# Performance work log

Measured on AMD Instinct MI355X. Metric: run time of the kernel, lower is better.

## Reference

```python
import jax, jax.numpy as jnp
import numpy as np

N_FFT = 1024
HOP = 256
B = 8
T = 2048  # n_frames
FREQ = N_FFT // 2 + 1


def setup_inputs() -> dict:
    key = jax.random.key(0)
    k1, k2 = jax.random.split(key)
    real_stft = jax.random.normal(k1, (B, 1, T, FREQ), dtype=jnp.float32)
    imag_stft = jax.random.normal(k2, (B, 1, T, FREQ), dtype=jnp.float32)
    # Build DFT synthesis matrices (same as torch module __init__, scaled=False)
    n = np.arange(N_FFT)
    hann = (0.5 - 0.5 * np.cos(2.0 * np.pi * n / N_FFT))  # fftbins=True hann
    ang = 2.0 * np.pi * np.outer(n, n) / N_FFT            # [k, n]
    W_real = (np.cos(ang) * hann[None, :] / N_FFT).astype(np.float32)
    W_imag = (np.sin(ang) * hann[None, :] / N_FFT).astype(np.float32)
    ola_window = (hann ** 2).astype(np.float32)
    return {
        "real_stft": real_stft,
        "imag_stft": imag_stft,
        "W_real": jnp.asarray(W_real),
        "W_imag": jnp.asarray(W_imag),
        "ola_window": jnp.asarray(ola_window),
    }


def reference(real_stft, imag_stft, W_real, W_imag, ola_window):
    n_fft = W_real.shape[0]
    b, _, n_frames, _ = real_stft.shape
    # (B, T, F) -> (B, F, T)
    fr = jnp.swapaxes(real_stft[:, 0], 1, 2)
    fi = jnp.swapaxes(imag_stft[:, 0], 1, 2)
    # Hermitian extension to full spectrum (B, n_fft, T)
    full_r = jnp.concatenate([fr, jnp.flip(fr[:, 1:-1, :], axis=1)], axis=1)
    full_i = jnp.concatenate([fi, -jnp.flip(fi[:, 1:-1, :], axis=1)], axis=1)
    # 1x1-conv DFT projection: out[b,t,n] = sum_k W[k,n] * x[b,k,t]
    frames = (jnp.einsum('kn,bkt->btn', W_real, full_r)
              - jnp.einsum('kn,bkt->btn', W_imag, full_i))  # (B, T, n_fft)
    out_len = (n_frames - 1) * HOP + n_fft
    # Overlap-add fold via scatter-add
    idx = (jnp.arange(n_frames)[:, None] * HOP + jnp.arange(n_fft)[None, :]).reshape(-1)
    y = jnp.zeros((b, out_len), frames.dtype).at[:, idx].add(frames.reshape(b, -1))
    # Window-sum fold + normalization
    wsum = jnp.zeros((out_len,), frames.dtype).at[idx].add(jnp.tile(ola_window, n_frames))
    wsum = jnp.clip(wsum, 1e-11, None)
    y = y / wsum[None, :]
    half = n_fft // 2
    return y[:, half:out_len - half]
```

## Files before the change

### kernel.cpp

```cpp
#include <hip/hip_runtime.h>


#define BATCH    8
#define NFRAMES  2048
#define FREQ     513
#define OUTCOLS  524032
#define FRAMES_B ((size_t)16384 * 1024 * 2)
#define TW_OFF   FRAMES_B
#define WS_NEED  (FRAMES_B + 1024 * 8)

#define PD(a) ((a) + ((a) >> 4))

typedef __attribute__((ext_vector_type(2))) float f32x2;

__device__ __forceinline__ unsigned short f2bf(float x) {
    unsigned u = __float_as_uint(x);
    return (unsigned short)((u + 0x7fffu + ((u >> 16) & 1u)) >> 16);
}

__global__ __launch_bounds__(256) void twiddle_prep(float* __restrict__ tw) {
    int k = blockIdx.x * 256 + threadIdx.x;
    float s, c;
    sincosf(6.283185307179586f * (float)k * (1.0f / 1024.0f), &s, &c);
    ((f32x2*)tw)[k] = (f32x2){c, s};
}

__global__ __launch_bounds__(256) void ifft_frames3(
    const float* __restrict__ re, const float* __restrict__ im,
    const float* __restrict__ ola, const float* __restrict__ twg,
    unsigned short* __restrict__ frames) {
    __shared__ f32x2 X[1088], Y[1088];

    const int blk = blockIdx.x;
    const int r0  = blk * 2;
    const int tid = threadIdx.x;
    const f32x2* tw = (const f32x2*)twg;

    const float* fre0 = re + (size_t)r0 * FREQ;
    const float* fim0 = im + (size_t)r0 * FREQ;
    const float* fre1 = fre0 + FREQ;
    const float* fim1 = fim0 + FREQ;
#pragma unroll
    for (int h = 0; h < 2; ++h) {
        int k = tid + 256 * h;
        float a1 = fre0[k], b1 = fim0[k];
        float a2 = fre1[k], b2 = fim1[k];
        if (k == 0) { b1 = 0.0f; b2 = 0.0f; }
        X[PD(k)] = (f32x2){a1 - b2, b1 + a2};
        if (k > 0) X[PD(1024 - k)] = (f32x2){a1 + b2, a2 - b1};
    }
    if (tid == 0)
        X[PD(512)] = (f32x2){fre0[512], fre1[512]};
    __syncthreads();

#define STAGE(S, RB, WB)                                                      \
    {                                                                         \
        const int p  = tid / (S);                                             \
        const int q  = tid % (S);                                             \
        f32x2 a = RB[PD(tid)];                                                \
        f32x2 b = RB[PD(tid + 256)];                                          \
        f32x2 c = RB[PD(tid + 512)];                                          \
        f32x2 d = RB[PD(tid + 768)];                                          \
        float apcr = a[0] + c[0], apci = a[1] + c[1];                         \
        float amcr = a[0] - c[0], amci = a[1] - c[1];                         \
        float bpdr = b[0] + d[0], bpdi = b[1] + d[1];                         \
        float jbr  = -(b[1] - d[1]), jbi = (b[0] - d[0]);        \
        const int t1 = p * (S);                                               \
        f32x2 w1 = tw[t1], w2 = tw[2 * t1], w3 = tw[3 * t1];                  \
        const int wb = 4 * (S) * p + q;                                       \
        WB[PD(wb)] = (f32x2){apcr + bpdr, apci + bpdi};                       \
        float u1r = amcr + jbr, u1i = amci + jbi;                             \
        WB[PD(wb + (S))]     = (f32x2){u1r * w1[0] - u1i * w1[1],             \
                                       u1r * w1[1] + u1i * w1[0]};            \
        float u2r = apcr - bpdr, u2i = apci - bpdi;                           \
        WB[PD(wb + 2 * (S))] = (f32x2){u2r * w2[0] - u2i * w2[1],             \
                                       u2r * w2[1] + u2i * w2[0]};            \
        float u3r = amcr - jbr, u3i = amci - jbi;                             \
        WB[PD(wb + 3 * (S))] = (f32x2){u3r * w3[0] - u3i * w3[1],             \
                                       u3r * w3[1] + u3i * w3[0]};            \
        __syncthreads();                                                      \
    }

    STAGE(1,  X, Y)
    STAGE(4,  Y, X)
    STAGE(16, X, Y)
    STAGE(64, Y, X)
    {
        f32x2 a = X[PD(tid)];
        f32x2 b = X[PD(tid + 256)];
        f32x2 c = X[PD(tid + 512)];
        f32x2 d = X[PD(tid + 768)];
        float apcr = a[0] + c[0], apci = a[1] + c[1];
        float amcr = a[0] - c[0], amci = a[1] - c[1];
        float bpdr = b[0] + d[0], bpdi = b[1] + d[1];
        float jbr  = -(b[1] - d[1]), jbi = (b[0] - d[0]);
        Y[PD(tid)]       = (f32x2){apcr + bpdr, apci + bpdi};
        Y[PD(tid + 256)] = (f32x2){amcr + jbr, amci + jbi};
        Y[PD(tid + 512)] = (f32x2){apcr - bpdr, apci - bpdi};
        Y[PD(tid + 768)] = (f32x2){amcr - jbr, amci - jbi};
        __syncthreads();
    }
#undef STAGE

    const float inv = 1.0f / 1024.0f;
    unsigned* f0 = (unsigned*)frames + (size_t)r0 * 512;
    unsigned* f1 = f0 + 512;
#pragma unroll
    for (int h = 0; h < 2; ++h) {
        int n = 2 * tid + 512 * h;
        f32x2 o  = *(const f32x2*)(ola + n);
        float s0 = sqrtf(o[0]) * inv, s1 = sqrtf(o[1]) * inv;
        f32x2 z0 = Y[PD(n)], z1 = Y[PD(n + 1)];
        f0[tid + 256 * h] = (unsigned)f2bf(z0[0] * s0) | ((unsigned)f2bf(z1[0] * s1) << 16);
        f1[tid + 256 * h] = (unsigned)f2bf(z0[1] * s0) | ((unsigned)f2bf(z1[1] * s1) << 16);
    }
}

__global__ __launch_bounds__(256) void ola_fold2(
    const unsigned short* __restrict__ frames, const float* __restrict__ ola,
    float* __restrict__ out) {
    const int col0 = (blockIdx.x * 256 + threadIdx.x) * 2;
    if (col0 >= OUTCOLS) return;
    const int b  = blockIdx.y;
    const int s  = col0 + 512;
    const int g  = s >> 8;
    const int ls = s & 255;

    float acc0 = 0.0f, acc1 = 0.0f, ws0 = 0.0f, ws1 = 0.0f;
#pragma unroll
    for (int j = 0; j < 4; ++j) {
        const int t = g - j;
        if (t >= 0 && t < NFRAMES) {
            unsigned u = *(const unsigned*)(frames + ((size_t)(b * NFRAMES + t) << 10) + ls + 256 * j);
            acc0 += __uint_as_float(u << 16);
            acc1 += __uint_as_float(u & 0xffff0000u);
            f32x2 o = *(const f32x2*)(ola + ls + 256 * j);
            ws0 += o[0];
            ws1 += o[1];
        }
    }
    ws0 = fmaxf(ws0, 1e-11f);
    ws1 = fmaxf(ws1, 1e-11f);
    *(f32x2*)(out + (size_t)b * OUTCOLS + col0) = (f32x2){acc0 / ws0, acc1 / ws1};
}

__global__ __launch_bounds__(256) void istft_naive(
    const float* __restrict__ re, const float* __restrict__ im,
    const float* __restrict__ Wr, const float* __restrict__ Wi,
    const float* __restrict__ ola, float* __restrict__ out) {
    const int g = blockIdx.x + 2, b = blockIdx.y, ls = threadIdx.x;
    __shared__ float s_fr[4][FREQ];
    __shared__ float s_fi[4][FREQ];
#pragma unroll
    for (int jj = 0; jj < 4; ++jj) {
        const int t = g - jj;
        const bool valid = (t >= 0 && t < NFRAMES);
        const size_t base = ((size_t)b * NFRAMES + (valid ? t : 0)) * FREQ;
        for (int k = ls; k < FREQ; k += 256) {
            const float f = (k == 0 || k == FREQ - 1) ? 1.0f : 2.0f;
            s_fr[jj][k] = valid ? re[base + k] * f : 0.0f;
            s_fi[jj][k] = valid ? im[base + k] * f : 0.0f;
        }
    }
    __syncthreads();
    const float* wr = Wr + ls;
    const float* wi = Wi + ls;
    float acc = 0.0f;
    for (int k = 0; k < FREQ; ++k) {
        const float* wrk = wr + (size_t)k * 1024;
        const float* wik = wi + (size_t)k * 1024;
#pragma unroll
        for (int jj = 0; jj < 4; ++jj) {
            acc = fmaf(wrk[jj * 256], s_fr[jj][k], acc);
            acc = fmaf(-wik[jj * 256], s_fi[jj][k], acc);
        }
    }
    float wsv = 0.0f;
#pragma unroll
    for (int jj = 0; jj < 4; ++jj) {
        const int t = g - jj;
        if (t >= 0 && t < NFRAMES) wsv += ola[ls + jj * 256];
    }
    wsv = fmaxf(wsv, 1e-11f);
    out[(size_t)b * OUTCOLS + (g * 256 + ls - 512)] = acc / wsv;
}

extern "C" void kernel_launch(void* const* d_in, const int* in_sizes, int n_in,
                              void* d_out, int out_size, void* d_ws, size_t ws_size,
                              hipStream_t stream) {
    const float* re  = (const float*)d_in[0];
    const float* im  = (const float*)d_in[1];
    const float* Wr  = (const float*)d_in[2];
    const float* Wi  = (const float*)d_in[3];
    const float* ola = (const float*)d_in[4];
    float* out = (float*)d_out;

    if (ws_size >= WS_NEED) {
        unsigned short* frames = (unsigned short*)d_ws;
        float* tw = (float*)((char*)d_ws + TW_OFF);
        hipLaunchKernelGGL(twiddle_prep, dim3(4), dim3(256), 0, stream, tw);
        hipLaunchKernelGGL(ifft_frames3, dim3(8192), dim3(256), 0, stream,
                           re, im, ola, tw, frames);
        hipLaunchKernelGGL(ola_fold2, dim3(1024, BATCH), dim3(256), 0, stream,
                           frames, ola, out);
    } else {
        dim3 grid(2047, BATCH);
        hipLaunchKernelGGL(istft_naive, grid, dim3(256), 0, stream,
                           re, im, Wr, Wi, ola, out);
    }
}
```

Measured before the change: 46.19 us.

## Fuse Hermitian load into first FFT stage, write output directly, widen OLA fold

The Hermitian-extension load now feeds the first radix-4 butterfly straight from registers, which removes one shared-memory round trip and a barrier. The final butterfly writes bf16 frame outputs directly instead of staging them through shared memory, also dropping a barrier. The overlap-add fold now handles four columns per thread with 8-byte and 16-byte vector loads and a half-size grid. Frame stores become 2-byte scattered writes instead of packed 4-byte writes, which may reduce store efficiency.

```diff
diff --git a/kernel.cpp b/kernel.cpp
--- a/kernel.cpp
+++ b/kernel.cpp
@@ -12,6 +12,8 @@
 #define PD(a) ((a) + ((a) >> 4))
 
 typedef __attribute__((ext_vector_type(2))) float f32x2;
+typedef __attribute__((ext_vector_type(4))) float f32x4;
+typedef __attribute__((ext_vector_type(2))) unsigned uint2v;
 
 __device__ __forceinline__ unsigned short f2bf(float x) {
     unsigned u = __float_as_uint(x);
@@ -25,14 +27,13 @@
     ((f32x2*)tw)[k] = (f32x2){c, s};
 }
 
-__global__ __launch_bounds__(256) void ifft_frames3(
+__global__ __launch_bounds__(256) void ifft_frames5(
     const float* __restrict__ re, const float* __restrict__ im,
     const float* __restrict__ ola, const float* __restrict__ twg,
     unsigned short* __restrict__ frames) {
     __shared__ f32x2 X[1088], Y[1088];
 
-    const int blk = blockIdx.x;
-    const int r0  = blk * 2;
+    const int r0  = blockIdx.x * 2;
     const int tid = threadIdx.x;
     const f32x2* tw = (const f32x2*)twg;
 
@@ -40,23 +41,54 @@
     const float* fim0 = im + (size_t)r0 * FREQ;
     const float* fre1 = fre0 + FREQ;
     const float* fim1 = fim0 + FREQ;
-#pragma unroll
-    for (int h = 0; h < 2; ++h) {
-        int k = tid + 256 * h;
-        float a1 = fre0[k], b1 = fim0[k];
-        float a2 = fre1[k], b2 = fim1[k];
-        if (k == 0) { b1 = 0.0f; b2 = 0.0f; }
-        X[PD(k)] = (f32x2){a1 - b2, b1 + a2};
-        if (k > 0) X[PD(1024 - k)] = (f32x2){a1 + b2, a2 - b1};
-    }
-    if (tid == 0)
-        X[PD(512)] = (f32x2){fre0[512], fre1[512]};
+
+    {
+        f32x2 a, b, c, d;
+        {
+            float A1 = fre0[tid], B1 = fim0[tid];
+            float A2 = fre1[tid], B2 = fim1[tid];
+            if (tid == 0) { B1 = 0.0f; B2 = 0.0f; }
+            a = (f32x2){A1 - B2, B1 + A2};
+        }
+        {
+            float A1 = fre0[tid + 256], B1 = fim0[tid + 256];
+            float A2 = fre1[tid + 256], B2 = fim1[tid + 256];
+            b = (f32x2){A1 - B2, B1 + A2};
+        }
+        {
+            int m = 512 - tid;
+            float A1 = fre0[m], B1 = fim0[m];
+            float A2 = fre1[m], B2 = fim1[m];
+            if (tid == 0) { B1 = 0.0f; B2 = 0.0f; }
+            c = (f32x2){A1 + B2, A2 - B1};
+        }
+        {
+            int m = 256 - tid;
+            float A1 = fre0[m], B1 = fim0[m];
+            float A2 = fre1[m], B2 = fim1[m];
+            d = (f32x2){A1 + B2, A2 - B1};
+        }
+        float apcr = a[0] + c[0], apci = a[1] + c[1];
+        float amcr = a[0] - c[0], amci = a[1] - c[1];
+        float bpdr = b[0] + d[0], bpdi = b[1] + d[1];
+        float jbr  = -(b[1] - d[1]), jbi = (b[0] - d[0]);
+        f32x2 w1 = tw[tid], w2 = tw[2 * tid], w3 = tw[3 * tid];
+        const int wb = 4 * tid;
+        Y[PD(wb)] = (f32x2){apcr + bpdr, apci + bpdi};
+        float u1r = amcr + jbr, u1i = amci + jbi;
+        Y[PD(wb + 1)] = (f32x2){u1r * w1[0] - u1i * w1[1], u1r * w1[1] + u1i * w1[0]};
+        float u2r = apcr - bpdr, u2i = apci - bpdi;
+        Y[PD(wb + 2)] = (f32x2){u2r * w2[0] - u2i * w2[1], u2r * w2[1] + u2i * w2[0]};
+        float u3r = amcr - jbr, u3i = amci - jbi;
+        Y[PD(wb + 3)] = (f32x2){u3r * w3[0] - u3i * w3[1], u3r * w3[1] + u3i * w3[0]};
+    }
     __syncthreads();
 
 #define STAGE(S, RB, WB)                                                      \
     {                                                                         \
-        const int p  = tid / (S);                                             \
-        const int q  = tid % (S);                                             \
+        const int S_ = (S);                                                   \
+        const int p  = tid / S_;                                              \
+        const int q  = tid - p * S_;                                          \
         f32x2 a = RB[PD(tid)];                                                \
         f32x2 b = RB[PD(tid + 256)];                                          \
         f32x2 c = RB[PD(tid + 512)];                                          \
@@ -65,26 +97,27 @@
         float amcr = a[0] - c[0], amci = a[1] - c[1];                         \
         float bpdr = b[0] + d[0], bpdi = b[1] + d[1];                         \
         float jbr  = -(b[1] - d[1]), jbi = (b[0] - d[0]);        \
-        const int t1 = p * (S);                                               \
+        const int t1 = p * S_;                                                \
         f32x2 w1 = tw[t1], w2 = tw[2 * t1], w3 = tw[3 * t1];                  \
-        const int wb = 4 * (S) * p + q;                                       \
+        const int wb = 4 * S_ * p + q;                                        \
         WB[PD(wb)] = (f32x2){apcr + bpdr, apci + bpdi};                       \
         float u1r = amcr + jbr, u1i = amci + jbi;                             \
-        WB[PD(wb + (S))]     = (f32x2){u1r * w1[0] - u1i * w1[1],             \
-                                       u1r * w1[1] + u1i * w1[0]};            \
+        WB[PD(wb + S_)]     = (f32x2){u1r * w1[0] - u1i * w1[1],              \
+                                      u1r * w1[1] + u1i * w1[0]};             \
         float u2r = apcr - bpdr, u2i = apci - bpdi;                           \
-        WB[PD(wb + 2 * (S))] = (f32x2){u2r * w2[0] - u2i * w2[1],             \
-                                       u2r * w2[1] + u2i * w2[0]};            \
+        WB[PD(wb + 2 * S_)] = (f32x2){u2r * w2[0] - u2i * w2[1],              \
+                                      u2r * w2[1] + u2i * w2[0]};             \
         float u3r = amcr - jbr, u3i = amci - jbi;                             \
-        WB[PD(wb + 3 * (S))] = (f32x2){u3r * w3[0] - u3i * w3[1],             \
-                                       u3r * w3[1] + u3i * w3[0]};            \
+        WB[PD(wb + 3 * S_)] = (f32x2){u3r * w3[0] - u3i * w3[1],              \
+                                      u3r * w3[1] + u3i * w3[0]};             \
         __syncthreads();                                                      \
     }
 
-    STAGE(1,  X, Y)
     STAGE(4,  Y, X)
     STAGE(16, X, Y)
     STAGE(64, Y, X)
+#undef STAGE
+
     {
         f32x2 a = X[PD(tid)];
         f32x2 b = X[PD(tid + 256)];
@@ -94,54 +127,53 @@
         float amcr = a[0] - c[0], amci = a[1] - c[1];
         float bpdr = b[0] + d[0], bpdi = b[1] + d[1];
         float jbr  = -(b[1] - d[1]), jbi = (b[0] - d[0]);
-        Y[PD(tid)]       = (f32x2){apcr + bpdr, apci + bpdi};
-        Y[PD(tid + 256)] = (f32x2){amcr + jbr, amci + jbi};
-        Y[PD(tid + 512)] = (f32x2){apcr - bpdr, apci - bpdi};
-        Y[PD(tid + 768)] = (f32x2){amcr - jbr, amci - jbi};
-        __syncthreads();
-    }
-#undef STAGE
-
-    const float inv = 1.0f / 1024.0f;
-    unsigned* f0 = (unsigned*)frames + (size_t)r0 * 512;
-    unsigned* f1 = f0 + 512;
-#pragma unroll
-    for (int h = 0; h < 2; ++h) {
-        int n = 2 * tid + 512 * h;
-        f32x2 o  = *(const f32x2*)(ola + n);
-        float s0 = sqrtf(o[0]) * inv, s1 = sqrtf(o[1]) * inv;
-        f32x2 z0 = Y[PD(n)], z1 = Y[PD(n + 1)];
-        f0[tid + 256 * h] = (unsigned)f2bf(z0[0] * s0) | ((unsigned)f2bf(z1[0] * s1) << 16);
-        f1[tid + 256 * h] = (unsigned)f2bf(z0[1] * s0) | ((unsigned)f2bf(z1[1] * s1) << 16);
-    }
-}
-
-__global__ __launch_bounds__(256) void ola_fold2(
+        f32x2 y0 = (f32x2){apcr + bpdr, apci + bpdi};
+        f32x2 y1 = (f32x2){amcr + jbr,  amci + jbi };
+        f32x2 y2 = (f32x2){apcr - bpdr, apci - bpdi};
+        f32x2 y3 = (f32x2){amcr - jbr,  amci - jbi };
+
+        const float inv = 1.0f / 1024.0f;
+        unsigned short* fR = frames + (size_t)r0 * 1024;
+        unsigned short* fI = fR + 1024;
+        float s0 = sqrtf(ola[tid])       * inv;
+        float s1 = sqrtf(ola[tid + 256]) * inv;
+        float s2 = sqrtf(ola[tid + 512]) * inv;
+        float s3 = sqrtf(ola[tid + 768]) * inv;
+        fR[tid]       = f2bf(y0[0] * s0);  fI[tid]       = f2bf(y0[1] * s0);
+        fR[tid + 256] = f2bf(y1[0] * s1);  fI[tid + 256] = f2bf(y1[1] * s1);
+        fR[tid + 512] = f2bf(y2[0] * s2);  fI[tid + 512] = f2bf(y2[1] * s2);
+        fR[tid + 768] = f2bf(y3[0] * s3);  fI[tid + 768] = f2bf(y3[1] * s3);
+    }
+}
+
+__global__ __launch_bounds__(256) void ola_fold4(
     const unsigned short* __restrict__ frames, const float* __restrict__ ola,
     float* __restrict__ out) {
-    const int col0 = (blockIdx.x * 256 + threadIdx.x) * 2;
+    const int col0 = (blockIdx.x * 256 + threadIdx.x) * 4;
     if (col0 >= OUTCOLS) return;
     const int b  = blockIdx.y;
     const int s  = col0 + 512;
     const int g  = s >> 8;
     const int ls = s & 255;
 
-    float acc0 = 0.0f, acc1 = 0.0f, ws0 = 0.0f, ws1 = 0.0f;
+    float a0 = 0.f, a1 = 0.f, a2 = 0.f, a3 = 0.f;
+    float w0 = 0.f, w1 = 0.f, w2 = 0.f, w3 = 0.f;
 #pragma unroll
     for (int j = 0; j < 4; ++j) {
         const int t = g - j;
         if (t >= 0 && t < NFRAMES) {
-            unsigned u = *(const unsigned*)(frames + ((size_t)(b * NFRAMES + t) << 10) + ls + 256 * j);
-            acc0 += __uint_as_float(u << 16);
-            acc1 += __uint_as_float(u & 0xffff0000u);
-            f32x2 o = *(const f32x2*)(ola + ls + 256 * j);
-            ws0 += o[0];
-            ws1 += o[1];
-        }
-    }
-    ws0 = fmaxf(ws0, 1e-11f);
-    ws1 = fmaxf(ws1, 1e-11f);
-    *(f32x2*)(out + (size_t)b * OUTCOLS + col0) = (f32x2){acc0 / ws0, acc1 / ws1};
+            uint2v u = *(const uint2v*)(frames + (((size_t)(b * NFRAMES + t)) << 10) + ls + 256 * j);
+            a0 += __uint_as_float(u[0] << 16);
+            a1 += __uint_as_float(u[0] & 0xffff0000u);
+            a2 += __uint_as_float(u[1] << 16);
+            a3 += __uint_as_float(u[1] & 0xffff0000u);
+            f32x4 o = *(const f32x4*)(ola + ls + 256 * j);
+            w0 += o[0]; w1 += o[1]; w2 += o[2]; w3 += o[3];
+        }
+    }
+    f32x4 r = (f32x4){a0 / fmaxf(w0, 1e-11f), a1 / fmaxf(w1, 1e-11f),
+                      a2 / fmaxf(w2, 1e-11f), a3 / fmaxf(w3, 1e-11f)};
+    *(f32x4*)(out + (size_t)b * OUTCOLS + col0) = r;
 }
 
 __global__ __launch_bounds__(256) void istft_naive(
@@ -199,9 +231,9 @@
         unsigned short* frames = (unsigned short*)d_ws;
         float* tw = (float*)((char*)d_ws + TW_OFF);
         hipLaunchKernelGGL(twiddle_prep, dim3(4), dim3(256), 0, stream, tw);
-        hipLaunchKernelGGL(ifft_frames3, dim3(8192), dim3(256), 0, stream,
+        hipLaunchKernelGGL(ifft_frames5, dim3(8192), dim3(256), 0, stream,
                            re, im, ola, tw, frames);
-        hipLaunchKernelGGL(ola_fold2, dim3(1024, BATCH), dim3(256), 0, stream,
+        hipLaunchKernelGGL(ola_fold4, dim3(512, BATCH), dim3(256), 0, stream,
                            frames, ola, out);
     } else {
         dim3 grid(2047, BATCH);
```

Measured after the change: 43.14 us. 6.6% less time.
